# Optimization experiments

Hardware: AMD Instinct MI355X
Metric: run time of the kernel (lower is better)

## Reference

```python
import jax, jax.numpy as jnp
import numpy as np

EPS = 1e-5
NUM_GROUPS = 32
NUM_HEADS = 4


def setup_inputs() -> dict:
    key = jax.random.key(0)
    k1, k2, k3 = jax.random.split(key, 3)
    b, c, h, w = 8, 256, 32, 32
    x = jax.random.normal(k1, (b, c, h, w), dtype=jnp.float32)
    gn_w = jnp.ones((c,), dtype=jnp.float32)
    gn_b = jnp.zeros((c,), dtype=jnp.float32)
    qkv_w = jax.random.normal(k2, (3 * c, c), dtype=jnp.float32) * (1.0 / np.sqrt(c))
    qkv_b = jnp.zeros((3 * c,), dtype=jnp.float32)
    proj_w = jax.random.normal(k3, (c, c), dtype=jnp.float32) * (1.0 / np.sqrt(c))
    proj_b = jnp.zeros((c,), dtype=jnp.float32)
    return {"x": x, "gn_w": gn_w, "gn_b": gn_b, "qkv_w": qkv_w,
            "qkv_b": qkv_b, "proj_w": proj_w, "proj_b": proj_b}


def _group_norm(x, weight, bias):
    # x: (b, c, n)
    b, c, n = x.shape
    xg = x.reshape(b, NUM_GROUPS, (c // NUM_GROUPS) * n)
    mean = jnp.mean(xg, axis=-1, keepdims=True)
    var = jnp.mean(jnp.square(xg - mean), axis=-1, keepdims=True)
    xn = ((xg - mean) * jax.lax.rsqrt(var + EPS)).reshape(b, c, n)
    return xn * weight[None, :, None] + bias[None, :, None]


def reference(x, gn_w, gn_b, qkv_w, qkv_b, proj_w, proj_b):
    b, c, h, w = x.shape
    # FFT2 over spatial dims, then view_as_real -> flatten: seq len N = 2*h*w
    xf = jnp.fft.fft2(x)                                   # (b,c,h,w) complex64
    xr = jnp.stack([xf.real, xf.imag], axis=-1).reshape(b, c, -1)  # (b,c,N)
    n = xr.shape[-1]
    # GroupNorm(32, c) then 1x1 Conv1d producing qkv
    normed = _group_norm(xr, gn_w, gn_b)
    qkv = jnp.einsum('oc,bcn->bon', qkv_w, normed) + qkv_b[None, :, None]  # (b,3c,N)
    # split heads exactly like torch: view(b*H, 3c/H, N) then split along dim 1
    qkv = qkv.reshape(b * NUM_HEADS, 3 * c // NUM_HEADS, n)
    ch = c // NUM_HEADS
    q, k, v = qkv[:, :ch], qkv[:, ch:2 * ch], qkv[:, 2 * ch:]
    scale = ch ** -0.25
    weight = jnp.einsum('bct,bcs->bts', q * scale, k * scale)  # (b*H, N, N)
    weight = jax.nn.softmax(weight, axis=-1)
    a = jnp.einsum('bts,bcs->bct', weight, v).reshape(b, c, n)
    out = jnp.einsum('oc,bcn->bon', proj_w, a) + proj_b[None, :, None]  # (b,c,N)
    # back to complex and IFFT2
    out = out.reshape(b, c, h, w, 2)
    oc = jax.lax.complex(out[..., 0], out[..., 1])
    res = jnp.fft.ifft2(oc)                                # (b,c,h,w) complex64
    # return complex result as real/imag pair
    return jnp.stack([res.real, res.imag], axis=-1)         # (b,c,h,w,2)
```

## Files before the change

### kernel.cpp

```cpp
#include <hip/hip_runtime.h>
#include <hip/hip_bf16.h>
#include <stdint.h>

#define PI_F 3.14159265358979323846f
#define C1_EXP 0.18033688f
#define C2_EXP 23.083120f

typedef __bf16 bf16x8 __attribute__((ext_vector_type(8)));
typedef float f32x4 __attribute__((ext_vector_type(4)));
typedef unsigned int uint32x4 __attribute__((ext_vector_type(4)));

#define BAR_LDS() asm volatile("s_waitcnt lgkmcnt(0)\n\ts_barrier" ::: "memory")

__device__ __forceinline__ bf16x8 neg8(bf16x8 v) {
  union { bf16x8 b; uint32x4 u; } x;
  x.b = v;
  x.u ^= (uint32x4){0x80008000u, 0x80008000u, 0x80008000u, 0x80008000u};
  return x.b;
}

#define MFMA3(acc, Ph, Pl, Qh, Ql)                                        \
  acc = __builtin_amdgcn_mfma_f32_16x16x32_bf16(Ph, Qh, acc, 0, 0, 0);    \
  acc = __builtin_amdgcn_mfma_f32_16x16x32_bf16(Ph, Ql, acc, 0, 0, 0);    \
  acc = __builtin_amdgcn_mfma_f32_16x16x32_bf16(Pl, Qh, acc, 0, 0, 0);

__device__ __forceinline__ int slot2n(int slot) {
  const int pi = slot >> 1, im = slot & 1;
  int k1, k2;
  if (pi < 480)      { k1 = 1 + (pi >> 5); k2 = pi & 31; }
  else if (pi < 495) { k1 = 0;  k2 = pi - 479; }
  else if (pi < 510) { k1 = 16; k2 = pi - 494; }
  else if (pi < 514) { k1 = ((pi - 510) >> 1) * 16; k2 = ((pi - 510) & 1) * 16; }
  else               { k1 = 0; k2 = 0; }
  return 2 * (k1 * 32 + k2) + im;
}

__device__ __forceinline__ void build_twiddle_lds(char* smem, int tid) {
  for (int e = tid; e < 1024; e += 256) {
    const int j = e >> 5, k = e & 31;
    const int t = (j * k) & 31;
    float sv, cv;
    sincosf(2.0f * PI_F * (float)t / 32.0f, &sv, &cv);
    const __bf16 ch = (__bf16)cv, sh = (__bf16)sv;
    *(__bf16*)(smem + j * 80 + k * 2) = ch;
    *(__bf16*)(smem + 2560 + j * 80 + k * 2) = (__bf16)(cv - (float)ch);
    *(__bf16*)(smem + 5120 + j * 80 + k * 2) = sh;
    *(__bf16*)(smem + 7680 + j * 80 + k * 2) = (__bf16)(sv - (float)sh);
  }
}

__global__ __launch_bounds__(256) void k_fft2(const float* __restrict__ x,
                                              float* __restrict__ xr,
                                              float* __restrict__ stats_part) {
  __shared__ __align__(16) char smem[51200];
  const int tid = threadIdx.x, lane = tid & 63, wv = tid >> 6;
  const int quad = lane >> 4, q16 = lane & 15;
  const int slice = blockIdx.x * 4 + wv;
  char* const wr_ = smem + 10240 + wv * 10240;

  const float* xs = x + (size_t)slice * 1024;
  float4 xv[4];
#pragma unroll
  for (int u = 0; u < 4; ++u) xv[u] = ((const float4*)xs)[u * 64 + lane];

  build_twiddle_lds(smem, tid);

#pragma unroll
  for (int u = 0; u < 4; ++u) {
    const int f = u * 64 + lane;
    const float4 v = xv[u];
    const int row = f >> 3, c4 = (f & 7) * 4;
    union { unsigned long long q; __bf16 b[4]; } ph, pl;
    ph.b[0] = (__bf16)v.x; ph.b[1] = (__bf16)v.y;
    ph.b[2] = (__bf16)v.z; ph.b[3] = (__bf16)v.w;
    pl.b[0] = (__bf16)(v.x - (float)ph.b[0]);
    pl.b[1] = (__bf16)(v.y - (float)ph.b[1]);
    pl.b[2] = (__bf16)(v.z - (float)ph.b[2]);
    pl.b[3] = (__bf16)(v.w - (float)ph.b[3]);
    *(unsigned long long*)(wr_ + row * 80 + c4 * 2) = ph.q;
    *(unsigned long long*)(wr_ + 2560 + row * 80 + c4 * 2) = pl.q;
  }
  __syncthreads();

  bf16x8 cch[2], ccl[2], ssh[2], ssl[2], xh[2], xl[2];
#pragma unroll
  for (int t2 = 0; t2 < 2; ++t2) {
    const int row = t2 * 16 + q16;
    cch[t2] = *(const bf16x8*)(smem + row * 80 + quad * 16);
    ccl[t2] = *(const bf16x8*)(smem + 2560 + row * 80 + quad * 16);
    ssh[t2] = *(const bf16x8*)(smem + 5120 + row * 80 + quad * 16);
    ssl[t2] = *(const bf16x8*)(smem + 7680 + row * 80 + quad * 16);
    xh[t2] = *(const bf16x8*)(wr_ + row * 80 + quad * 16);
    xl[t2] = *(const bf16x8*)(wr_ + 2560 + row * 80 + quad * 16);
  }

  f32x4 yre[2][2] = {}, yim[2][2] = {};
#pragma unroll
  for (int mt = 0; mt < 2; ++mt)
#pragma unroll
    for (int nt = 0; nt < 2; ++nt) {
      MFMA3(yre[mt][nt], xh[mt], xl[mt], cch[nt], ccl[nt]);
      MFMA3(yim[mt][nt], xh[mt], xl[mt], ssh[nt], ssl[nt]);
    }

#pragma unroll
  for (int mt = 0; mt < 2; ++mt)
#pragma unroll
    for (int nt = 0; nt < 2; ++nt) {
      char* base = wr_ + (nt * 16 + q16) * 80 + (mt * 16 + quad * 4) * 2;
      union { unsigned long long q; __bf16 b[4]; } h, l;
#pragma unroll
      for (int r = 0; r < 4; ++r) {
        const float v = yre[mt][nt][r];
        h.b[r] = (__bf16)v; l.b[r] = (__bf16)(v - (float)h.b[r]);
      }
      *(unsigned long long*)(base) = h.q;
      *(unsigned long long*)(base + 2560) = l.q;
#pragma unroll
      for (int r = 0; r < 4; ++r) {
        const float v = -yim[mt][nt][r];
        h.b[r] = (__bf16)v; l.b[r] = (__bf16)(v - (float)h.b[r]);
      }
      *(unsigned long long*)(base + 5120) = h.q;
      *(unsigned long long*)(base + 7680) = l.q;
    }
  asm volatile("" ::: "memory");

  bf16x8 yreh[2], yrel[2], yimh[2], yiml[2];
#pragma unroll
  for (int nt = 0; nt < 2; ++nt) {
    const int row = nt * 16 + q16;
    yreh[nt] = *(const bf16x8*)(wr_ + row * 80 + quad * 16);
    yrel[nt] = *(const bf16x8*)(wr_ + 2560 + row * 80 + quad * 16);
    yimh[nt] = *(const bf16x8*)(wr_ + 5120 + row * 80 + quad * 16);
    yiml[nt] = *(const bf16x8*)(wr_ + 7680 + row * 80 + quad * 16);
  }

  f32x4 zre[2][2] = {}, zim[2][2] = {};
  bf16x8 ssnh[2], ssnl[2];
  ssnh[0] = neg8(ssh[0]); ssnh[1] = neg8(ssh[1]);
  ssnl[0] = neg8(ssl[0]); ssnl[1] = neg8(ssl[1]);
#pragma unroll
  for (int mt = 0; mt < 2; ++mt)
#pragma unroll
    for (int nt = 0; nt < 2; ++nt) {
      MFMA3(zre[mt][nt], cch[mt], ccl[mt], yreh[nt], yrel[nt]);
      MFMA3(zre[mt][nt], ssh[mt], ssl[mt], yimh[nt], yiml[nt]);
      MFMA3(zim[mt][nt], cch[mt], ccl[mt], yimh[nt], yiml[nt]);
      MFMA3(zim[mt][nt], ssnh[mt], ssnl[mt], yreh[nt], yrel[nt]);
    }

  float* op = xr + (size_t)slice * 2048;
  float s1 = 0.f, s2 = 0.f;
#pragma unroll
  for (int mt = 0; mt < 2; ++mt)
#pragma unroll
    for (int nt = 0; nt < 2; ++nt)
#pragma unroll
      for (int r = 0; r < 4; ++r) {
        const int k1 = mt * 16 + quad * 4 + r;
        const int k2 = nt * 16 + q16;
        const float a = zre[mt][nt][r], bimg = zim[mt][nt][r];
        s1 += a + bimg;
        s2 += a * a + bimg * bimg;
        float2 st; st.x = a; st.y = bimg;
        *(float2*)(op + 2 * (k1 * 32 + k2)) = st;
      }
#pragma unroll
  for (int off = 1; off <= 32; off <<= 1) {
    s1 += __shfl_xor(s1, off);
    s2 += __shfl_xor(s2, off);
  }
  if (lane == 0) {
    const int bg = (slice >> 8) * 32 + ((slice & 255) >> 3);
    const int sub = slice & 7;
    float2 st; st.x = s1; st.y = s2;
    *(float2*)(stats_part + (size_t)(bg * 8 + sub) * 2) = st;
  }
}

__global__ __launch_bounds__(256) void k_uvec(const float* __restrict__ stats_part,
                                              const float* __restrict__ gn_w,
                                              const float* __restrict__ gn_b,
                                              const float* __restrict__ qkv_w,
                                              const float* __restrict__ qkv_b,
                                              float* __restrict__ uk,
                                              float* __restrict__ uv) {
  const int blk = blockIdx.x;
  const int tid = threadIdx.x;
  const int b = blk >> 3, h = (blk >> 1) & 3, role = blk & 1;
  __shared__ float Bsh[256];
  {
    const int g = tid >> 3;
    float S = 0.f, S2 = 0.f;
#pragma unroll
    for (int s = 0; s < 8; ++s) {
      S  += stats_part[((b * 32 + g) * 8 + s) * 2];
      S2 += stats_part[((b * 32 + g) * 8 + s) * 2 + 1];
    }
    const float mean = S * (1.0f / 16384.0f);
    const float var = S2 * (1.0f / 16384.0f) - mean * mean;
    const float rstd = rsqrtf(var + 1e-5f);
    Bsh[tid] = gn_b[tid] - mean * rstd * gn_w[tid];
  }
  __syncthreads();
  const int cp = tid >> 2, seg = tid & 3;
  const int row = h * 192 + 64 + role * 64 + cp;
  const float* wr_ = qkv_w + (size_t)row * 256 + seg * 64;
  const float* bs = Bsh + seg * 64;
  float s = 0.f;
#pragma unroll
  for (int i = 0; i < 16; ++i) {
    const float4 w4 = *(const float4*)(wr_ + i * 4);
    const float4 b4 = *(const float4*)(bs + i * 4);
    s += w4.x * b4.x + w4.y * b4.y + w4.z * b4.z + w4.w * b4.w;
  }
  s += __shfl_xor(s, 1);
  s += __shfl_xor(s, 2);
  if (seg == 0) {
    float* dst = (role == 0) ? uk : uv;
    dst[(size_t)(b * 4 + h) * 64 + cp] = s + qkv_b[row];
  }
}

__global__ __launch_bounds__(256) void k_gntrans(const float* __restrict__ xr,
                                                 const float* __restrict__ stats_part,
                                                 const float* __restrict__ w,
                                                 const float* __restrict__ bias,
                                                 __bf16* __restrict__ xt) {
  const int n0 = blockIdx.x * 64;
  const int c0 = blockIdx.y * 64;
  const int b = blockIdx.z;
  __shared__ __bf16 Lt[64][72];
  __shared__ float gsum[8][2];
  const int tid = threadIdx.x;
  if (tid < 8) {
    const int g = (c0 >> 3) + tid;
    float S = 0.f, S2 = 0.f;
#pragma unroll
    for (int s = 0; s < 8; ++s) {
      S  += stats_part[((b * 32 + g) * 8 + s) * 2];
      S2 += stats_part[((b * 32 + g) * 8 + s) * 2 + 1];
    }
    gsum[tid][0] = S;
    gsum[tid][1] = S2;
  }
  __syncthreads();
  for (int i = tid; i < 1024; i += 256) {
    const int cl = i >> 4, c = c0 + cl, nl = (i & 15) * 4;
    const float S = gsum[cl >> 3][0];
    const float S2 = gsum[cl >> 3][1];
    const float mean = S * (1.0f / 16384.0f);
    const float var = S2 * (1.0f / 16384.0f) - mean * mean;
    const float rstd = rsqrtf(var + 1e-5f);
    const float sc = rstd * w[c];
    const float sh = bias[c] - mean * sc;
    const float4 v = *(const float4*)(xr + ((size_t)b * 256 + c) * 2048 + n0 + nl);
    Lt[nl][cl] = (__bf16)(v.x * sc + sh);
    Lt[nl + 1][cl] = (__bf16)(v.y * sc + sh);
    Lt[nl + 2][cl] = (__bf16)(v.z * sc + sh);
    Lt[nl + 3][cl] = (__bf16)(v.w * sc + sh);
  }
  __syncthreads();
  __bf16* dst = xt + (size_t)b * 524288 + (size_t)n0 * 256 + c0;
  for (int i = tid; i < 512; i += 256) {
    const int nl = i >> 3, cch = (i & 7) * 8;
    *(uint4*)(dst + (size_t)nl * 256 + cch) = *(const uint4*)&Lt[nl][cch];
  }
}

__global__ __launch_bounds__(256) void k_gemm_qkv(const float* __restrict__ W,
                                                  const __bf16* __restrict__ X,
                                                  const float* __restrict__ bias,
                                                  const float* __restrict__ uk,
                                                  float* __restrict__ dq,
                                                  __bf16* __restrict__ Qt,
                                                  __bf16* __restrict__ Kt,
                                                  __bf16* __restrict__ Vt) {
  const int tx = blockIdx.x;
  const int b = blockIdx.y;
  int role, hd, nt;
  if (tx < 64) { role = 0; hd = tx >> 4; nt = tx & 15; }
  else if (tx < 100) { role = 1; const int i = tx - 64; hd = i / 9; nt = i - hd * 9; }
  else { role = 2; const int i = tx - 100; hd = i / 9; nt = i - hd * 9; }
  const int n0 = nt * 128;
  const int bo = hd * 192 + role * 64;
  const __bf16* Xb = X + (size_t)b * 524288;

  __shared__ __align__(16) char smem[30720];
  __bf16 (*Ot)[72] = (__bf16(*)[72])smem;
  __bf16 (*Ot2)[136] = (__bf16(*)[136])smem;

  const int tid = threadIdx.x, lane = tid & 63, wv = tid >> 6;
  const int quad = lane >> 4, q16 = lane & 15, wn = wv * 32;

  const int rowA = tid >> 2, chA = (tid & 3) * 8;
  const int browB0 = tid >> 2, bchB = (tid & 3) * 8;
  const float* wA = W + (size_t)(bo + rowA) * 256 + chA;

  const int s0r = n0 + browB0, s1r = n0 + browB0 + 64;
  const int pn0 = (role == 0) ? s0r : slot2n(s0r);
  const int pn1 = (role == 0) ? s1r : slot2n(s1r);

  float4 aP0 = *(const float4*)(wA);
  float4 aP1 = *(const float4*)(wA + 4);
  uint4 bP0 = *(const uint4*)(Xb + (size_t)pn0 * 256 + bchB);
  uint4 bP1 = *(const uint4*)(Xb + (size_t)pn1 * 256 + bchB);

  f32x4 acc[4][2] = {};
  int bsel = 0;
  for (int k0 = 0; k0 < 256; k0 += 32) {
    char* const Ab = smem + bsel;
    char* const Bb = smem + bsel + 5120;
    {
      union { uint4 u; __bf16 h[8]; } pa;
      pa.h[0] = (__bf16)aP0.x; pa.h[1] = (__bf16)aP0.y;
      pa.h[2] = (__bf16)aP0.z; pa.h[3] = (__bf16)aP0.w;
      pa.h[4] = (__bf16)aP1.x; pa.h[5] = (__bf16)aP1.y;
      pa.h[6] = (__bf16)aP1.z; pa.h[7] = (__bf16)aP1.w;
      *(uint4*)(Ab + rowA * 80 + chA * 2) = pa.u;
      *(uint4*)(Bb + browB0 * 80 + bchB * 2) = bP0;
      *(uint4*)(Bb + (browB0 + 64) * 80 + bchB * 2) = bP1;
    }
    __syncthreads();
    if (k0 + 32 < 256) {
      const int kn = k0 + 32;
      aP0 = *(const float4*)(wA + kn);
      aP1 = *(const float4*)(wA + kn + 4);
      bP0 = *(const uint4*)(Xb + (size_t)pn0 * 256 + kn + bchB);
      bP1 = *(const uint4*)(Xb + (size_t)pn1 * 256 + kn + bchB);
    }
    bf16x8 af[4], bfr[2];
#pragma unroll
    for (int mt = 0; mt < 4; ++mt)
      af[mt] = *(const bf16x8*)(Ab + (mt * 16 + q16) * 80 + quad * 16);
#pragma unroll
    for (int jn = 0; jn < 2; ++jn)
      bfr[jn] = *(const bf16x8*)(Bb + (wn + jn * 16 + q16) * 80 + quad * 16);
#pragma unroll
    for (int mt = 0; mt < 4; ++mt)
#pragma unroll
      for (int jn = 0; jn < 2; ++jn)
        acc[mt][jn] = __builtin_amdgcn_mfma_f32_16x16x32_bf16(af[mt], bfr[jn], acc[mt][jn], 0, 0, 0);
    bsel ^= 15360;
  }
  __syncthreads();

  const int bh = b * 4 + hd;
  if (role == 2) {
#pragma unroll
    for (int mt = 0; mt < 4; ++mt)
#pragma unroll
      for (int r = 0; r < 4; ++r) {
        const int c = mt * 16 + quad * 4 + r;
        const float bv = bias[bo + c];
#pragma unroll
        for (int jn = 0; jn < 2; ++jn)
          Ot2[c][wn + jn * 16 + q16] = (__bf16)(acc[mt][jn][r] + bv);
      }
    __syncthreads();
    __bf16* dst = Vt + (size_t)bh * 73728;
    for (int i = tid; i < 1024; i += 256) {
      const int c = i >> 4, sg = (i & 15) * 8;
      *(uint4*)(dst + (size_t)c * 1152 + n0 + sg) = *(const uint4*)&Ot2[c][sg];
    }
  } else {
    __bf16* dst = (role == 0 ? Qt + (size_t)bh * 131072
                             : Kt + (size_t)bh * 73728);
#pragma unroll
    for (int mt = 0; mt < 4; ++mt)
#pragma unroll
      for (int r = 0; r < 4; ++r) {
        const int c = mt * 16 + quad * 4 + r;
        const float bv = bias[bo + c];
#pragma unroll
        for (int jn = 0; jn < 2; ++jn)
          Ot[wn + jn * 16 + q16][c] = (__bf16)(acc[mt][jn][r] + bv);
      }
    __syncthreads();
    for (int i = tid; i < 1024; i += 256) {
      const int nl = i >> 3, cch = (i & 7) * 8;
      *(uint4*)(dst + (size_t)(n0 + nl) * 64 + cch) = *(const uint4*)&Ot[nl][cch];
    }
    if (role == 0 && tid < 128) {
      const float* ukp = uk + (size_t)bh * 64;
      float dv = 0.f;
#pragma unroll
      for (int g8 = 0; g8 < 8; ++g8) {
        const bf16x8 qv = *(const bf16x8*)&Ot[tid][g8 * 8];
#pragma unroll
        for (int k = 0; k < 8; ++k) dv += (float)qv[k] * ukp[g8 * 8 + k];
      }
      dq[(size_t)bh * 2048 + n0 + tid] = dv * (2.0f * C1_EXP);
    }
  }
}

template <bool EDGE>
__device__ __forceinline__ void attn_iter(
    const int s0, const int send, const int quad,
    const __bf16* __restrict__ kg, const __bf16* __restrict__ vg,
    char* const kw, char* const vw,
    const char* const (&krp)[2][2], const char* const (&vrp)[4],
    char* const (&pwp)[2][2], const char* const (&prp)[2],
    const bf16x8 (&bq)[2][2], const float (&Dm)[2],
    uint4& kA, uint4& vA, f32x4 (&oacc)[2][4],
    float (&lsum)[2], float (&spsum)[2]) {
  *(uint4*)kw = kA;
  *(uint4*)vw = vA;
  BAR_LDS();
  if (s0 + 32 < send) {
    kA = *(const uint4*)(kg + (size_t)(s0 + 32) * 64);
    vA = *(const uint4*)(vg + s0 + 32);
  }

  f32x4 sacc[2][2] = {};
#pragma unroll
  for (int j = 0; j < 2; ++j)
#pragma unroll
    for (int kk = 0; kk < 2; ++kk) {
      const bf16x8 ak = *(const bf16x8*)krp[j][kk];
      sacc[0][j] = __builtin_amdgcn_mfma_f32_16x16x32_bf16(ak, bq[0][kk], sacc[0][j], 0, 0, 0);
      sacc[1][j] = __builtin_amdgcn_mfma_f32_16x16x32_bf16(ak, bq[1][kk], sacc[1][j], 0, 0, 0);
    }

#pragma unroll
  for (int b = 0; b < 2; ++b) {
    float lacc = 0.f, spacc = 0.f;
#pragma unroll
    for (int j = 0; j < 2; ++j) {
      float B0, B2, Bv1, Bv3, Bm1, Bm3;
      if (EDGE) {
        const int sg = s0 + j * 16 + quad * 4;
        B0 = (sg < 1020) ? (1.0f - C2_EXP) : ((sg < 1028) ? -C2_EXP : -1e30f);
        B2 = (sg + 2 < 1020) ? (1.0f - C2_EXP)
                             : ((sg + 2 < 1028) ? -C2_EXP : -1e30f);
        Bv1 = (sg + 1 < 1028) ? -C2_EXP : -1e30f;
        Bv3 = (sg + 3 < 1028) ? -C2_EXP : -1e30f;
        Bm1 = (sg + 1 < 1020) ? Dm[b] : -1e30f;
        Bm3 = (sg + 3 < 1020) ? Dm[b] : -1e30f;
      } else {
        B0 = 1.0f - C2_EXP;
        B2 = 1.0f - C2_EXP;
        Bv1 = -C2_EXP;
        Bv3 = -C2_EXP;
        Bm1 = Dm[b];
        Bm3 = Dm[b];
      }
      const float P0  = __builtin_amdgcn_exp2f(fmaf(sacc[b][j][0],  C1_EXP, B0));
      const float Pv1 = __builtin_amdgcn_exp2f(fmaf(sacc[b][j][1],  C1_EXP, Bv1));
      const float P2  = __builtin_amdgcn_exp2f(fmaf(sacc[b][j][2],  C1_EXP, B2));
      const float Pv3 = __builtin_amdgcn_exp2f(fmaf(sacc[b][j][3],  C1_EXP, Bv3));
      const float pm1 = __builtin_amdgcn_exp2f(fmaf(sacc[b][j][1], -C1_EXP, Bm1));
      const float pm3 = __builtin_amdgcn_exp2f(fmaf(sacc[b][j][3], -C1_EXP, Bm3));
      const float mm = pm1 + pm3;
      lacc += (P0 + P2) + (Pv1 + Pv3) + mm;
      spacc += mm;
      union { uint2 u; __bf16 h[4]; } pk;
      pk.h[0] = (__bf16)P0;
      pk.h[1] = (__bf16)(Pv1 - pm1);
      pk.h[2] = (__bf16)P2;
      pk.h[3] = (__bf16)(Pv3 - pm3);
      *(uint2*)pwp[b][j] = pk.u;
    }
    lsum[b] += lacc;
    spsum[b] += spacc;
  }
  asm volatile("" ::: "memory");

  bf16x8 bp[2];
  bp[0] = *(const bf16x8*)prp[0];
  bp[1] = *(const bf16x8*)prp[1];
#pragma unroll
  for (int jc = 0; jc < 4; ++jc) {
    const bf16x8 av = *(const bf16x8*)vrp[jc];
    oacc[0][jc] = __builtin_amdgcn_mfma_f32_16x16x32_bf16(av, bp[0], oacc[0][jc], 0, 0, 0);
    oacc[1][jc] = __builtin_amdgcn_mfma_f32_16x16x32_bf16(av, bp[1], oacc[1][jc], 0, 0, 0);
  }
  BAR_LDS();
}

__global__ __launch_bounds__(256, 4) void k_attn_mfma(const __bf16* __restrict__ Qt,
                                                      const __bf16* __restrict__ Kt,
                                                      const __bf16* __restrict__ Vt,
                                                      const float* __restrict__ dq,
                                                      const float* __restrict__ uv,
                                                      __bf16* __restrict__ opart) {
  const int t0 = blockIdx.x * 128;
  const int bh = blockIdx.y;
  const __bf16* kt = Kt + (size_t)bh * 73728;
  const __bf16* vt = Vt + (size_t)bh * 73728;

  __shared__ __align__(16) char smem[16384];

  const int tid = threadIdx.x, lane = tid & 63, wv = tid >> 6;
  const int quad = lane >> 4, q16 = lane & 15;
  const int wband = wv * 32;

  const int rK = tid >> 3, gK = tid & 7;
  char* const kw = smem + rK * 128 + ((gK ^ (rK & 7)) * 16);
  const int cV = tid >> 2, gV = tid & 3;
  char* const vw = smem + 4096 + (cV >> 1) * 128 +
                   ((((cV & 1) * 4 + gV) ^ ((cV >> 1) & 7)) * 16);
  const __bf16* const kg = kt + (size_t)rK * 64 + gK * 8;
  const __bf16* const vg = vt + (size_t)cV * 1152 + gV * 8;

  const char* krp[2][2];
#pragma unroll
  for (int j = 0; j < 2; ++j)
#pragma unroll
    for (int kk = 0; kk < 2; ++kk)
      krp[j][kk] = smem + (j * 16 + q16) * 128 + (((kk * 4 + quad) ^ (q16 & 7)) * 16);
  const int a7 = (q16 >> 1) & 7, p1 = q16 & 1;
  const char* vrp[4];
#pragma unroll
  for (int jc = 0; jc < 4; ++jc)
    vrp[jc] = smem + 4096 + (jc * 8 + (q16 >> 1)) * 128 +
              (((p1 * 4 + quad) ^ a7) * 16);
  char* pwp[2][2];
  const char* prp[2];
#pragma unroll
  for (int b = 0; b < 2; ++b) {
    const int mrow = ((wband + b * 16) >> 1) + (q16 >> 1);
    prp[b] = smem + 8192 + mrow * 128 + (((p1 * 4 + quad) ^ a7) * 16);
#pragma unroll
    for (int j = 0; j < 2; ++j)
      pwp[b][j] = smem + 8192 + mrow * 128 +
                  (((p1 * 4 + j * 2 + (quad >> 1)) ^ a7) * 16) + (quad & 1) * 8;
  }

  const __bf16* qbase = Qt + (size_t)bh * 131072;
  bf16x8 bq[2][2];
  float Dm[2];
#pragma unroll
  for (int b = 0; b < 2; ++b) {
    const int t = t0 + wband + b * 16 + q16;
    const __bf16* qp = qbase + (size_t)t * 64 + quad * 8;
    bq[b][0] = *(const bf16x8*)qp;
    bq[b][1] = *(const bf16x8*)(qp + 32);
    Dm[b] = dq[(size_t)bh * 2048 + t] - C2_EXP;
  }

  f32x4 oacc[2][4] = {};
  float lsum[2] = {0.f, 0.f};
  float spsum[2] = {0.f, 0.f};

  const int send = 1056;
  uint4 kA = *(const uint4*)(kg);
  uint4 vA = *(const uint4*)(vg);

  for (int s0 = 0; s0 < 992; s0 += 32)
    attn_iter<false>(s0, send, quad, kg, vg, kw, vw, krp, vrp, pwp, prp,
                     bq, Dm, kA, vA, oacc, lsum, spsum);
  for (int s0 = 992; s0 < send; s0 += 32)
    attn_iter<true>(s0, send, quad, kg, vg, kw, vw, krp, vrp, pwp, prp,
                    bq, Dm, kA, vA, oacc, lsum, spsum);

  float4 uv4[4];
  {
    const float* uvp = uv + (size_t)bh * 64;
#pragma unroll
    for (int jc = 0; jc < 4; ++jc)
      uv4[jc] = *(const float4*)(uvp + jc * 16 + quad * 4);
  }

#pragma unroll
  for (int b = 0; b < 2; ++b) {
    float l = lsum[b], sp = spsum[b];
    l += __shfl_xor(l, 16);
    l += __shfl_xor(l, 32);
    sp += __shfl_xor(sp, 16);
    sp += __shfl_xor(sp, 32);
    const float inv = 1.0f / l;
    const float su = 2.0f * sp * inv;
    const int t = t0 + wband + b * 16 + q16;
    __bf16* opp = opart + ((size_t)bh * 2048 + t) * 64;
#pragma unroll
    for (int jc = 0; jc < 4; ++jc) {
      union { uint2 u; __bf16 h[4]; } pk;
      pk.h[0] = (__bf16)(oacc[b][jc][0] * inv + su * uv4[jc].x);
      pk.h[1] = (__bf16)(oacc[b][jc][1] * inv + su * uv4[jc].y);
      pk.h[2] = (__bf16)(oacc[b][jc][2] * inv + su * uv4[jc].z);
      pk.h[3] = (__bf16)(oacc[b][jc][3] * inv + su * uv4[jc].w);
      *(uint2*)(opp + jc * 16 + quad * 4) = pk.u;
    }
  }
}

__global__ __launch_bounds__(256) void k_gemm_proj(const float* __restrict__ W,
                                                   const __bf16* __restrict__ opart,
                                                   const float* __restrict__ bias,
                                                   float* __restrict__ C) {
  const int n0 = blockIdx.x * 128;
  const int bo = blockIdx.y * 64;
  const int b = blockIdx.z;
  float* Cb = C + (size_t)b * 524288;

  __shared__ __align__(16) char smem[30720];

  const int tid = threadIdx.x, lane = tid & 63, wv = tid >> 6;
  const int quad = lane >> 4, q16 = lane & 15, wn = wv * 32;

  const int rowA = tid >> 2, chA = (tid & 3) * 8;
  const int browB0 = tid >> 2, bchB = (tid & 3) * 8;
  const float* wA = W + (size_t)(bo + rowA) * 256 + chA;

  float4 aP0 = *(const float4*)(wA);
  float4 aP1 = *(const float4*)(wA + 4);
  uint4 oPd[2];
#pragma unroll
  for (int g = 0; g < 2; ++g) {
    const int t = n0 + browB0 + g * 64;
    const size_t rr = (size_t)(b * 4) * 2048 + t;
    oPd[g] = *(const uint4*)(opart + rr * 64 + bchB);
  }

  f32x4 acc[4][2] = {};
  int bsel = 0;
  for (int k0 = 0; k0 < 256; k0 += 32) {
    char* const Ab = smem + bsel;
    char* const Bb = smem + bsel + 5120;
    {
      union { uint4 u; __bf16 h[8]; } pa;
      pa.h[0] = (__bf16)aP0.x; pa.h[1] = (__bf16)aP0.y;
      pa.h[2] = (__bf16)aP0.z; pa.h[3] = (__bf16)aP0.w;
      pa.h[4] = (__bf16)aP1.x; pa.h[5] = (__bf16)aP1.y;
      pa.h[6] = (__bf16)aP1.z; pa.h[7] = (__bf16)aP1.w;
      *(uint4*)(Ab + rowA * 80 + chA * 2) = pa.u;
      *(uint4*)(Bb + browB0 * 80 + bchB * 2) = oPd[0];
      *(uint4*)(Bb + (browB0 + 64) * 80 + bchB * 2) = oPd[1];
    }
    __syncthreads();
    if (k0 + 32 < 256) {
      const int kn = k0 + 32;
      aP0 = *(const float4*)(wA + kn);
      aP1 = *(const float4*)(wA + kn + 4);
      const int c = kn + bchB;
      const int hd = c >> 6, cu = c & 63;
#pragma unroll
      for (int g = 0; g < 2; ++g) {
        const int t = n0 + browB0 + g * 64;
        const size_t rr = (size_t)(b * 4 + hd) * 2048 + t;
        oPd[g] = *(const uint4*)(opart + rr * 64 + cu);
      }
    }
    bf16x8 af[4], bfr[2];
#pragma unroll
    for (int mt = 0; mt < 4; ++mt)
      af[mt] = *(const bf16x8*)(Ab + (mt * 16 + q16) * 80 + quad * 16);
#pragma unroll
    for (int jn = 0; jn < 2; ++jn)
      bfr[jn] = *(const bf16x8*)(Bb + (wn + jn * 16 + q16) * 80 + quad * 16);
#pragma unroll
    for (int mt = 0; mt < 4; ++mt)
#pragma unroll
      for (int jn = 0; jn < 2; ++jn)
        acc[mt][jn] = __builtin_amdgcn_mfma_f32_16x16x32_bf16(af[mt], bfr[jn], acc[mt][jn], 0, 0, 0);
    bsel ^= 15360;
  }

#pragma unroll
  for (int mt = 0; mt < 4; ++mt)
#pragma unroll
    for (int r = 0; r < 4; ++r) {
      const int o = bo + mt * 16 + quad * 4 + r;
      const float bv = bias[o];
#pragma unroll
      for (int jn = 0; jn < 2; ++jn)
        Cb[(size_t)o * 2048 + n0 + wn + jn * 16 + q16] = acc[mt][jn][r] + bv;
    }
}

__global__ __launch_bounds__(256) void k_ifft2(const float* __restrict__ spec,
                                               float* __restrict__ out) {
  __shared__ __align__(16) char smem[51200];
  const int tid = threadIdx.x, lane = tid & 63, wv = tid >> 6;
  const int quad = lane >> 4, q16 = lane & 15;
  const int slice = blockIdx.x * 4 + wv;
  char* const wr_ = smem + 10240 + wv * 10240;

  const float* sp = spec + (size_t)slice * 2048;
  float4 sv8[8];
#pragma unroll
  for (int u = 0; u < 8; ++u) sv8[u] = ((const float4*)sp)[u * 64 + lane];

  build_twiddle_lds(smem, tid);

#pragma unroll
  for (int u = 0; u < 8; ++u) {
    const int f = u * 64 + lane;
    const float4 v = sv8[u];
    const int k1 = f >> 4, k2 = (f & 15) * 2;
    char* base = wr_ + k1 * 80 + k2 * 2;
    union { unsigned int w; __bf16 b[2]; } p;
    const __bf16 rh0 = (__bf16)v.x, rh1 = (__bf16)v.z;
    const __bf16 ih0 = (__bf16)v.y, ih1 = (__bf16)v.w;
    p.b[0] = rh0; p.b[1] = rh1; *(unsigned int*)(base) = p.w;
    p.b[0] = (__bf16)(v.x - (float)rh0);
    p.b[1] = (__bf16)(v.z - (float)rh1); *(unsigned int*)(base + 2560) = p.w;
    p.b[0] = ih0; p.b[1] = ih1; *(unsigned int*)(base + 5120) = p.w;
    p.b[0] = (__bf16)(v.y - (float)ih0);
    p.b[1] = (__bf16)(v.w - (float)ih1); *(unsigned int*)(base + 7680) = p.w;
  }
  __syncthreads();

  bf16x8 cch[2], ccl[2], ssh[2], ssl[2], ssnh[2], ssnl[2];
  bf16x8 xreh[2], xrel[2], ximh[2], ximl[2];
#pragma unroll
  for (int t2 = 0; t2 < 2; ++t2) {
    const int row = t2 * 16 + q16;
    cch[t2] = *(const bf16x8*)(smem + row * 80 + quad * 16);
    ccl[t2] = *(const bf16x8*)(smem + 2560 + row * 80 + quad * 16);
    ssh[t2] = *(const bf16x8*)(smem + 5120 + row * 80 + quad * 16);
    ssl[t2] = *(const bf16x8*)(smem + 7680 + row * 80 + quad * 16);
    xreh[t2] = *(const bf16x8*)(wr_ + row * 80 + quad * 16);
    xrel[t2] = *(const bf16x8*)(wr_ + 2560 + row * 80 + quad * 16);
    ximh[t2] = *(const bf16x8*)(wr_ + 5120 + row * 80 + quad * 16);
    ximl[t2] = *(const bf16x8*)(wr_ + 7680 + row * 80 + quad * 16);
  }
  ssnh[0] = neg8(ssh[0]); ssnh[1] = neg8(ssh[1]);
  ssnl[0] = neg8(ssl[0]); ssnl[1] = neg8(ssl[1]);

  f32x4 yre[2][2] = {}, yim[2][2] = {};
#pragma unroll
  for (int mt = 0; mt < 2; ++mt)
#pragma unroll
    for (int nt = 0; nt < 2; ++nt) {
      MFMA3(yre[mt][nt], xreh[mt], xrel[mt], cch[nt], ccl[nt]);
      MFMA3(yre[mt][nt], ximh[mt], ximl[mt], ssnh[nt], ssnl[nt]);
      MFMA3(yim[mt][nt], xreh[mt], xrel[mt], ssh[nt], ssl[nt]);
      MFMA3(yim[mt][nt], ximh[mt], ximl[mt], cch[nt], ccl[nt]);
    }

#pragma unroll
  for (int mt = 0; mt < 2; ++mt)
#pragma unroll
    for (int nt = 0; nt < 2; ++nt) {
      char* base = wr_ + (nt * 16 + q16) * 80 + (mt * 16 + quad * 4) * 2;
      union { unsigned long long q; __bf16 b[4]; } h, l;
#pragma unroll
      for (int r = 0; r < 4; ++r) {
        const float v = yre[mt][nt][r];
        h.b[r] = (__bf16)v; l.b[r] = (__bf16)(v - (float)h.b[r]);
      }
      *(unsigned long long*)(base) = h.q;
      *(unsigned long long*)(base + 2560) = l.q;
#pragma unroll
      for (int r = 0; r < 4; ++r) {
        const float v = yim[mt][nt][r];
        h.b[r] = (__bf16)v; l.b[r] = (__bf16)(v - (float)h.b[r]);
      }
      *(unsigned long long*)(base + 5120) = h.q;
      *(unsigned long long*)(base + 7680) = l.q;
    }
  asm volatile("" ::: "memory");

  bf16x8 yreh[2], yrel[2], yimh[2], yiml[2];
#pragma unroll
  for (int nt = 0; nt < 2; ++nt) {
    const int row = nt * 16 + q16;
    yreh[nt] = *(const bf16x8*)(wr_ + row * 80 + quad * 16);
    yrel[nt] = *(const bf16x8*)(wr_ + 2560 + row * 80 + quad * 16);
    yimh[nt] = *(const bf16x8*)(wr_ + 5120 + row * 80 + quad * 16);
    yiml[nt] = *(const bf16x8*)(wr_ + 7680 + row * 80 + quad * 16);
  }

  f32x4 zre[2][2] = {}, zim[2][2] = {};
#pragma unroll
  for (int mt = 0; mt < 2; ++mt)
#pragma unroll
    for (int nt = 0; nt < 2; ++nt) {
      MFMA3(zre[mt][nt], cch[mt], ccl[mt], yreh[nt], yrel[nt]);
      MFMA3(zre[mt][nt], ssnh[mt], ssnl[mt], yimh[nt], yiml[nt]);
      MFMA3(zim[mt][nt], cch[mt], ccl[mt], yimh[nt], yiml[nt]);
      MFMA3(zim[mt][nt], ssh[mt], ssl[mt], yreh[nt], yrel[nt]);
    }

  float* op = out + (size_t)slice * 2048;
#pragma unroll
  for (int mt = 0; mt < 2; ++mt)
#pragma unroll
    for (int nt = 0; nt < 2; ++nt)
#pragma unroll
      for (int r = 0; r < 4; ++r) {
        const int n1 = mt * 16 + quad * 4 + r;
        const int n2 = nt * 16 + q16;
        float2 st;
        st.x = zre[mt][nt][r] * (1.0f / 1024.0f);
        st.y = zim[mt][nt][r] * (1.0f / 1024.0f);
        *(float2*)(op + 2 * (n1 * 32 + n2)) = st;
      }
}

extern "C" void kernel_launch(void* const* d_in, const int* in_sizes, int n_in,
                              void* d_out, int out_size, void* d_ws, size_t ws_size,
                              hipStream_t stream) {
  (void)in_sizes; (void)n_in; (void)out_size; (void)ws_size;
  const float* x      = (const float*)d_in[0];
  const float* gn_w   = (const float*)d_in[1];
  const float* gn_b   = (const float*)d_in[2];
  const float* qkv_w  = (const float*)d_in[3];
  const float* qkv_b  = (const float*)d_in[4];
  const float* proj_w = (const float*)d_in[5];
  const float* proj_b = (const float*)d_in[6];
  float* out = (float*)d_out;

  float* spec  = (float*)d_ws;
  __bf16* Qt   = (__bf16*)(spec + 4194304);
  __bf16* Kt   = Qt + 4194304;
  __bf16* Vt   = Kt + 2359296;
  float* xr    = (float*)(Vt + 2359296) + 512;
  __bf16* xt   = (__bf16*)(xr + 4194304);
  __bf16* opart = (__bf16*)xr;
  float*  dq    = (float*)(opart + 12582912);
  float*  uk    = dq + 65536;
  float*  uv    = uk + 2048;
  float*  stats_part = uv + 2048;

  k_fft2<<<512, 256, 0, stream>>>(x, xr, stats_part);
  k_uvec<<<64, 256, 0, stream>>>(stats_part, gn_w, gn_b, qkv_w, qkv_b, uk, uv);
  k_gntrans<<<dim3(32, 4, 8), 256, 0, stream>>>(xr, stats_part, gn_w, gn_b, xt);
  k_gemm_qkv<<<dim3(136, 8), 256, 0, stream>>>(qkv_w, xt, qkv_b, uk, dq,
                                               Qt, Kt, Vt);
  k_attn_mfma<<<dim3(16, 32), 256, 0, stream>>>(Qt, Kt, Vt, dq, uv, opart);
  k_gemm_proj<<<dim3(16, 4, 8), 256, 0, stream>>>(proj_w, opart, proj_b, spec);
  k_ifft2<<<512, 256, 0, stream>>>(spec, out);
}
```

Baseline: 158.4 us.

## Process 64 keys per barrier round in attention with doubled K/V staging

The attention main loop now stages two 32-key K/V tiles into a larger shared-memory buffer per round and runs two compute halves between barriers, instead of one tile per barrier pair. Each round also prefetches two tiles from global memory. The intent is to halve the number of workgroup barriers and give global loads more latency cover. The cost is a larger LDS footprint (16 KB to 24 KB per block), which could limit occupancy, and a hand-written, peeled tail for the last keys.

```diff
diff --git a/kernel.cpp b/kernel.cpp
--- a/kernel.cpp
+++ b/kernel.cpp
@@ -396,30 +396,19 @@
   }
 }
 
-template <bool EDGE>
-__device__ __forceinline__ void attn_iter(
-    const int s0, const int send, const int quad,
-    const __bf16* __restrict__ kg, const __bf16* __restrict__ vg,
-    char* const kw, char* const vw,
+template <bool EDGE, int OFF>
+__device__ __forceinline__ void attn_half(
+    const int s0, const int quad,
     const char* const (&krp)[2][2], const char* const (&vrp)[4],
     char* const (&pwp)[2][2], const char* const (&prp)[2],
     const bf16x8 (&bq)[2][2], const float (&Dm)[2],
-    uint4& kA, uint4& vA, f32x4 (&oacc)[2][4],
-    float (&lsum)[2], float (&spsum)[2]) {
-  *(uint4*)kw = kA;
-  *(uint4*)vw = vA;
-  BAR_LDS();
-  if (s0 + 32 < send) {
-    kA = *(const uint4*)(kg + (size_t)(s0 + 32) * 64);
-    vA = *(const uint4*)(vg + s0 + 32);
-  }
-
+    f32x4 (&oacc)[2][4], float (&lsum)[2], float (&spsum)[2]) {
   f32x4 sacc[2][2] = {};
 #pragma unroll
   for (int j = 0; j < 2; ++j)
 #pragma unroll
     for (int kk = 0; kk < 2; ++kk) {
-      const bf16x8 ak = *(const bf16x8*)krp[j][kk];
+      const bf16x8 ak = *(const bf16x8*)(krp[j][kk] + OFF);
       sacc[0][j] = __builtin_amdgcn_mfma_f32_16x16x32_bf16(ak, bq[0][kk], sacc[0][j], 0, 0, 0);
       sacc[1][j] = __builtin_amdgcn_mfma_f32_16x16x32_bf16(ak, bq[1][kk], sacc[1][j], 0, 0, 0);
     }
@@ -473,11 +462,10 @@
   bp[1] = *(const bf16x8*)prp[1];
 #pragma unroll
   for (int jc = 0; jc < 4; ++jc) {
-    const bf16x8 av = *(const bf16x8*)vrp[jc];
+    const bf16x8 av = *(const bf16x8*)(vrp[jc] + OFF);
     oacc[0][jc] = __builtin_amdgcn_mfma_f32_16x16x32_bf16(av, bp[0], oacc[0][jc], 0, 0, 0);
     oacc[1][jc] = __builtin_amdgcn_mfma_f32_16x16x32_bf16(av, bp[1], oacc[1][jc], 0, 0, 0);
   }
-  BAR_LDS();
 }
 
 __global__ __launch_bounds__(256, 4) void k_attn_mfma(const __bf16* __restrict__ Qt,
@@ -491,7 +479,7 @@
   const __bf16* kt = Kt + (size_t)bh * 73728;
   const __bf16* vt = Vt + (size_t)bh * 73728;
 
-  __shared__ __align__(16) char smem[16384];
+  __shared__ __align__(16) char smem[24576];
 
   const int tid = threadIdx.x, lane = tid & 63, wv = tid >> 6;
   const int quad = lane >> 4, q16 = lane & 15;
@@ -500,7 +488,7 @@
   const int rK = tid >> 3, gK = tid & 7;
   char* const kw = smem + rK * 128 + ((gK ^ (rK & 7)) * 16);
   const int cV = tid >> 2, gV = tid & 3;
-  char* const vw = smem + 4096 + (cV >> 1) * 128 +
+  char* const vw = smem + 8192 + (cV >> 1) * 128 +
                    ((((cV & 1) * 4 + gV) ^ ((cV >> 1) & 7)) * 16);
   const __bf16* const kg = kt + (size_t)rK * 64 + gK * 8;
   const __bf16* const vg = vt + (size_t)cV * 1152 + gV * 8;
@@ -515,17 +503,17 @@
   const char* vrp[4];
 #pragma unroll
   for (int jc = 0; jc < 4; ++jc)
-    vrp[jc] = smem + 4096 + (jc * 8 + (q16 >> 1)) * 128 +
+    vrp[jc] = smem + 8192 + (jc * 8 + (q16 >> 1)) * 128 +
               (((p1 * 4 + quad) ^ a7) * 16);
   char* pwp[2][2];
   const char* prp[2];
 #pragma unroll
   for (int b = 0; b < 2; ++b) {
     const int mrow = ((wband + b * 16) >> 1) + (q16 >> 1);
-    prp[b] = smem + 8192 + mrow * 128 + (((p1 * 4 + quad) ^ a7) * 16);
+    prp[b] = smem + 16384 + mrow * 128 + (((p1 * 4 + quad) ^ a7) * 16);
 #pragma unroll
     for (int j = 0; j < 2; ++j)
-      pwp[b][j] = smem + 8192 + mrow * 128 +
+      pwp[b][j] = smem + 16384 + mrow * 128 +
                   (((p1 * 4 + j * 2 + (quad >> 1)) ^ a7) * 16) + (quad & 1) * 8;
   }
 
@@ -545,16 +533,47 @@
   float lsum[2] = {0.f, 0.f};
   float spsum[2] = {0.f, 0.f};
 
-  const int send = 1056;
-  uint4 kA = *(const uint4*)(kg);
-  uint4 vA = *(const uint4*)(vg);
-
-  for (int s0 = 0; s0 < 992; s0 += 32)
-    attn_iter<false>(s0, send, quad, kg, vg, kw, vw, krp, vrp, pwp, prp,
-                     bq, Dm, kA, vA, oacc, lsum, spsum);
-  for (int s0 = 992; s0 < send; s0 += 32)
-    attn_iter<true>(s0, send, quad, kg, vg, kw, vw, krp, vrp, pwp, prp,
-                    bq, Dm, kA, vA, oacc, lsum, spsum);
+  uint4 kA0 = *(const uint4*)(kg);
+  uint4 kA1 = *(const uint4*)(kg + (size_t)32 * 64);
+  uint4 vA0 = *(const uint4*)(vg);
+  uint4 vA1 = *(const uint4*)(vg + 32);
+
+  int s0 = 0;
+#pragma unroll 1
+  for (int it = 0; it < 15; ++it) {
+    *(uint4*)kw = kA0;
+    *(uint4*)(kw + 4096) = kA1;
+    *(uint4*)vw = vA0;
+    *(uint4*)(vw + 4096) = vA1;
+    BAR_LDS();
+    kA0 = *(const uint4*)(kg + (size_t)(s0 + 64) * 64);
+    kA1 = *(const uint4*)(kg + (size_t)(s0 + 96) * 64);
+    vA0 = *(const uint4*)(vg + s0 + 64);
+    vA1 = *(const uint4*)(vg + s0 + 96);
+    attn_half<false, 0>(s0, quad, krp, vrp, pwp, prp, bq, Dm,
+                        oacc, lsum, spsum);
+    attn_half<false, 4096>(s0 + 32, quad, krp, vrp, pwp, prp, bq, Dm,
+                           oacc, lsum, spsum);
+    BAR_LDS();
+    s0 += 64;
+  }
+  *(uint4*)kw = kA0;
+  *(uint4*)(kw + 4096) = kA1;
+  *(uint4*)vw = vA0;
+  *(uint4*)(vw + 4096) = vA1;
+  BAR_LDS();
+  kA0 = *(const uint4*)(kg + (size_t)1024 * 64);
+  vA0 = *(const uint4*)(vg + 1024);
+  attn_half<false, 0>(960, quad, krp, vrp, pwp, prp, bq, Dm,
+                      oacc, lsum, spsum);
+  attn_half<true, 4096>(992, quad, krp, vrp, pwp, prp, bq, Dm,
+                        oacc, lsum, spsum);
+  BAR_LDS();
+  *(uint4*)kw = kA0;
+  *(uint4*)vw = vA0;
+  BAR_LDS();
+  attn_half<true, 0>(1024, quad, krp, vrp, pwp, prp, bq, Dm,
+                     oacc, lsum, spsum);
 
   float4 uv4[4];
   {
```

After: 155.8 us. Within noise of the previous version (-1.6%).
